# Performance work log

Measured on AMD Instinct MI355X. Metric: run time of the kernel, lower is better.

## Reference

```python
import jax, jax.numpy as jnp
import numpy as np

G = 8        # groups
GP = 8       # group_planes = out_planes // groups
K = 56       # kernel_size (attention axis length)
OP = 64      # out_planes
EPS = 1e-5   # BatchNorm eps (torch default)


def _bn(x, g, b, axes):
    # training-mode BatchNorm: batch statistics over `axes`, channel dim is axis 1
    m = x.mean(axes, keepdims=True)
    v = x.var(axes, keepdims=True)
    sh = [1] * x.ndim
    sh[1] = -1
    return (x - m) / jnp.sqrt(v + EPS) * g.reshape(sh) + b.reshape(sh)


def setup_inputs() -> dict:
    key = jax.random.key(0)
    k0, k1, k2 = jax.random.split(key, 3)
    x = jax.random.normal(k0, (1, 64, 32, 56, 32), jnp.float32)
    w_qkv = jax.random.normal(k1, (128, 64), jnp.float32) * (1.0 / 8.0)  # N(0, sqrt(1/in_planes))
    relative = jax.random.normal(k2, (16, 111), jnp.float32) * float(np.sqrt(1.0 / GP))
    return {
        "x": x,
        "w_qkv": w_qkv,
        "bn_qkv_g": jnp.ones(128, jnp.float32),
        "bn_qkv_b": jnp.zeros(128, jnp.float32),
        "bn_sim_g": jnp.ones(24, jnp.float32),
        "bn_sim_b": jnp.zeros(24, jnp.float32),
        "bn_out_g": jnp.ones(128, jnp.float32),
        "bn_out_b": jnp.zeros(128, jnp.float32),
        "relative": relative,
    }


def reference(x, w_qkv, bn_qkv_g, bn_qkv_b, bn_sim_g, bn_sim_b, bn_out_g, bn_out_b, relative):
    # get_input(x, 'x'): [N, C, D1, K, D2] -> [N, D1, D2, C, K]
    xp = jnp.transpose(x, (0, 2, 4, 1, 3))
    N, seq, W, C, Kk = xp.shape
    B = N * seq * W
    xb = xp.reshape(B, C, Kk)

    # 1x1 conv (qkv_transform) + BN1d
    qkv = jnp.einsum('oc,bck->bok', w_qkv, xb)            # [B, 2*OP, K]
    qkv = _bn(qkv, bn_qkv_g, bn_qkv_b, (0, 2))
    qkv = qkv.reshape(B, G, GP * 2, Kk)
    q, k, v = qkv[:, :, :GP // 2], qkv[:, :, GP // 2:GP], qkv[:, :, GP:]

    # relative position embeddings gathered from [2*GP, 2K-1] table
    qi = jnp.arange(K)[None, :]
    ki = jnp.arange(K)[:, None]
    flat = (ki - qi + K - 1).reshape(-1)
    emb = relative[:, flat].reshape(GP * 2, K, K)
    q_emb, k_emb, v_emb = emb[:GP // 2], emb[GP // 2:GP], emb[GP:]

    qr = jnp.einsum('bgci,cij->bgij', q, q_emb)
    kr = jnp.einsum('bgci,cij->bgij', k, k_emb).transpose(0, 1, 3, 2)
    qk = jnp.einsum('bgci,bgcj->bgij', q, k)

    ss = jnp.concatenate([qk, qr, kr], axis=1)            # [B, 3G, K, K]
    ss = _bn(ss, bn_sim_g, bn_sim_b, (0, 2, 3))
    sim = ss.reshape(B, 3, G, K, K).sum(axis=1)           # [B, G, K, K]
    sim = jax.nn.softmax(sim, axis=3)

    sv = jnp.einsum('bgij,bgcj->bgci', sim, v)            # [B, G, GP, K]
    sve = jnp.einsum('bgij,cij->bgci', sim, v_emb)        # [B, G, GP, K]
    so = jnp.concatenate([sv, sve], axis=-1).reshape(B, OP * 2, Kk)
    out = _bn(so, bn_out_g, bn_out_b, (0, 2))
    out = out.reshape(N, seq, W, OP, 2, Kk).sum(axis=-2)  # [N, seq, W, OP, K]

    # get_output(output, 'x'): [N, seq, W, OP, K] -> [N, OP, seq, K, W]
    return jnp.transpose(out, (0, 3, 1, 4, 2))
```

## Files before the change

### kernel.cpp

```cpp
#include <hip/hip_runtime.h>
#include <math.h>

#define EPS 1e-5f

typedef float f32x2 __attribute__((ext_vector_type(2)));
typedef float f32x4 __attribute__((ext_vector_type(4)));
__device__ __forceinline__ f32x2 fma2(f32x2 a, f32x2 b, f32x2 c) {
    return __builtin_elementwise_fma(a, b, c);
}
__device__ __forceinline__ f32x4 fma4(f32x4 a, f32x4 b, f32x4 c) {
    return __builtin_elementwise_fma(a, b, c);
}
__device__ __forceinline__ f32x2 sp2(float x) { f32x2 r = {x, x}; return r; }

__device__ __forceinline__ float dpp_add_shl(float v, int n) {
    int x;
    switch (n) {
        case 1: x = __builtin_amdgcn_mov_dpp(__float_as_int(v), 0x101, 0xF, 0xF, true); break;
        case 2: x = __builtin_amdgcn_mov_dpp(__float_as_int(v), 0x102, 0xF, 0xF, true); break;
        case 4: x = __builtin_amdgcn_mov_dpp(__float_as_int(v), 0x104, 0xF, 0xF, true); break;
        default: x = __builtin_amdgcn_mov_dpp(__float_as_int(v), 0x108, 0xF, 0xF, true); break;
    }
    return v + __int_as_float(x);
}
__device__ __forceinline__ float row_sum16(float v) {
    v = dpp_add_shl(v, 1);
    v = dpp_add_shl(v, 2);
    v = dpp_add_shl(v, 4);
    v = dpp_add_shl(v, 8);
    return v;
}


__global__ __launch_bounds__(256) void k_qkv2(const float* __restrict__ x,
                                              const float* __restrict__ w,
                                              const float* __restrict__ rel,
                                              float* __restrict__ qkv,
                                              float* __restrict__ P,
                                              float* __restrict__ tab) {
    __shared__ __align__(16) float X[64 * 256];
    __shared__ float T[8 * 264];
    const int t = threadIdx.x;

    if (blockIdx.x == 448) {
        float* r = X;
        for (int idx = t; idx < 444; idx += 256)
            *(float4*)&r[idx * 4] = *(const float4*)&rel[idx * 4];
        __syncthreads();
        for (int o = t; o < 2240; o += 256) {
            int row = o / 56, i = o - row * 56;
            float s = 0.f;
            if (row < 8) {
                const float* rr = &r[row * 111];
#pragma unroll
                for (int u = 0; u < 56; ++u) s += rr[i + u];
            } else if (row < 24) {
                int p = row - 8;
                const float* ra = &r[(p >> 2) * 111];
                const float* rb = &r[(p & 3) * 111];
#pragma unroll
                for (int u = 0; u < 56; ++u) s = fmaf(ra[i + u], rb[i + u], s);
            } else {
                int p = row - 24;
                const float* ra = &r[(4 + (p >> 2)) * 111];
                const float* rb = &r[(4 + (p & 3)) * 111];
#pragma unroll
                for (int u = 0; u < 56; ++u) s = fmaf(ra[i + u], rb[i + u], s);
            }
            tab[o] = s;
        }
        for (int o = t; o < 888; o += 256) {
            int c = o / 111, u = o - c * 111;
            tab[2240 + o] = rel[888 + c * 111 + 110 - u];
        }
        return;
    }

    const int tile = blockIdx.x % 224;
    const int half = blockIdx.x / 224;
    const int m0 = tile << 8;
    const int s = m0 / 1792;
    const int i0 = (m0 - s * 1792) >> 5;

    const float* xb = x + m0;
#pragma unroll
    for (int j = 0; j < 16; ++j) {
        int f = (j << 8) + t;
        int c = f >> 6, col = (f & 63) << 2;
        *(float4*)&X[(c << 8) + col] = *(const float4*)&xb[(size_t)c * 57344 + col];
    }
    __syncthreads();

    float* qb = qkv + (size_t)s * 229376 + i0;

    for (int oc = half * 8; oc < half * 8 + 8; ++oc) {
        const int o0 = oc << 3;
        const float* wp = w + (o0 << 6);
        f32x2 a01 = {0, 0}, a23 = {0, 0}, a45 = {0, 0}, a67 = {0, 0};
        for (int c = 0; c < 64; ++c) {
            float xv = X[(c << 8) + t];
            f32x2 w01 = {wp[c], wp[64 + c]};
            f32x2 w23 = {wp[128 + c], wp[192 + c]};
            f32x2 w45 = {wp[256 + c], wp[320 + c]};
            f32x2 w67 = {wp[384 + c], wp[448 + c]};
            f32x2 xs = sp2(xv);
            a01 = fma2(w01, xs, a01);
            a23 = fma2(w23, xs, a23);
            a45 = fma2(w45, xs, a45);
            a67 = fma2(w67, xs, a67);
        }
        float accv[8] = {a01.x, a01.y, a23.x, a23.y, a45.x, a45.y, a67.x, a67.y};
        __syncthreads();
#pragma unroll
        for (int k = 0; k < 8; ++k) T[k * 264 + t + (t >> 5)] = accv[k];
        __syncthreads();
#pragma unroll
        for (int e = 0; e < 8; ++e) {
            int flat = (e << 8) + t;
            int wcol = flat >> 6, oo = (flat >> 3) & 7, il = flat & 7;
            int mm = (il << 5) + wcol;
            qb[(size_t)wcol * 7168 + (o0 + oo) * 56 + il] = T[oo * 264 + mm + (mm >> 5)];
        }
        {
            int row = t >> 5, part = t & 31;
            float s1 = 0.f, s2 = 0.f;
#pragma unroll
            for (int e = 0; e < 8; ++e) {
                int mm = (part << 3) + e;
                float v = T[row * 264 + mm + (mm >> 5)];
                s1 += v; s2 += v * v;
            }
            s1 = row_sum16(s1);
            s2 = row_sum16(s2);
            s1 += __shfl_xor(s1, 16);
            s2 += __shfl_xor(s2, 16);
            if (part == 0) {
                P[(o0 + row) * 224 + tile] = s1;
                P[(128 + o0 + row) * 224 + tile] = s2;
            }
        }
    }
}

__global__ __launch_bounds__(256) void k_fin_red(const float* __restrict__ P,
                                                 const float* __restrict__ g,
                                                 const float* __restrict__ bb,
                                                 float* __restrict__ prm,
                                                 int nch, int npart, float invN) {
    __shared__ float rd[8];
    const int c = blockIdx.x, t = threadIdx.x;
    const float* r1 = P + (size_t)c * npart;
    const float* r2 = P + (size_t)(nch + c) * npart;
    float s1 = 0.f, s2 = 0.f;
    for (int p = t; p < npart; p += 256) { s1 += r1[p]; s2 += r2[p]; }
#pragma unroll
    for (int off = 32; off > 0; off >>= 1) { s1 += __shfl_xor(s1, off); s2 += __shfl_xor(s2, off); }
    if ((t & 63) == 0) { rd[t >> 6] = s1; rd[4 + (t >> 6)] = s2; }
    __syncthreads();
    if (t == 0) {
        s1 = rd[0] + rd[1] + rd[2] + rd[3];
        s2 = rd[4] + rd[5] + rd[6] + rd[7];
        float m = s1 * invN;
        float v = s2 * invN - m * m;
        float sc = g[c] * rsqrtf(v + EPS);
        prm[c] = sc;
        prm[nch + c] = bb[c] - m * sc;
    }
}

__global__ void k_fin(const float* __restrict__ sums, const float* __restrict__ g,
                      const float* __restrict__ bb, float* __restrict__ prm,
                      int nch, float invN) {
    int c = threadIdx.x;
    if (c >= nch) return;
    float m = sums[c] * invN;
    float v = sums[nch + c] * invN - m * m;
    float sc = g[c] * rsqrtf(v + EPS);
    prm[c] = sc;
    prm[nch + c] = bb[c] - m * sc;
}

__global__ __launch_bounds__(256) void k_sim3(const float* __restrict__ qkv,
                                              const float* __restrict__ prmQ,
                                              const float* __restrict__ tab,
                                              float* __restrict__ P) {
    __shared__ __align__(16) float qn[64 * 60];
    __shared__ __align__(16) float T[40 * 60];
    __shared__ float red[8 * 6];
    const int t = threadIdx.x, b = blockIdx.x;

    const float* span = qkv + (size_t)b * 7168;
    for (int idx = t; idx < 896; idx += 256) {
        int e0 = idx * 4;
        int g = e0 / 448, r = e0 - g * 448, c = r / 56, i = r - c * 56;
        int ch = g * 16 + c;
        float sc = prmQ[ch], sh = prmQ[128 + ch];
        float4 vv = *(const float4*)&span[g * 896 + r];
        float4 o;
        o.x = vv.x * sc + sh; o.y = vv.y * sc + sh;
        o.z = vv.z * sc + sh; o.w = vv.w * sc + sh;
        *(float4*)&qn[(g * 8 + c) * 60 + i] = o;
    }
    for (int idx = t; idx < 560; idx += 256) {
        int e0 = idx * 4;
        int row = e0 / 56, i = e0 - row * 56;
        int lr = (row < 8) ? (32 + row) : (row - 8);
        *(float4*)&T[lr * 60 + i] = *(const float4*)&tab[e0];
    }
    __syncthreads();

    const int g = t >> 5, u = t & 31;
    const int half = (u < 16) ? 0 : 4;
    const float* rowA = &qn[g * 480 + (half + ((u >> 2) & 3)) * 60];
    const float* rowB = &qn[g * 480 + (half + (u & 3)) * 60];
    const float* tabS = &T[u * 60];
    const float* tabR = &T[(32 + half + (u & 3)) * 60];

    f32x4 gram4 = {0, 0, 0, 0}, wgt4 = {0, 0, 0, 0};
    f32x4 lin14 = {0, 0, 0, 0}, lin24 = {0, 0, 0, 0};
#pragma unroll
    for (int i = 0; i < 56; i += 4) {
        f32x4 a = *(const f32x4*)&rowA[i];
        f32x4 b2 = *(const f32x4*)&rowB[i];
        f32x4 p = a * b2;
        gram4 += p;
        wgt4 = fma4(p, *(const f32x4*)&tabS[i], wgt4);
        lin14 += b2;
        lin24 = fma4(b2, *(const f32x4*)&tabR[i], lin24);
    }
    float gram = (gram4.x + gram4.y) + (gram4.z + gram4.w);
    float wgt = (wgt4.x + wgt4.y) + (wgt4.z + wgt4.w);
    float lin1 = (lin14.x + lin14.y) + (lin14.z + lin14.w);
    float lin2 = (lin24.x + lin24.y) + (lin24.z + lin24.w);

    float linP = __shfl_xor(lin1, 16);
    float gramP = __shfl_xor(gram, 16);
    float v0 = (u < 4) ? lin1 * linP : 0.f;
    float v1 = (u < 16) ? gram * gramP : 0.f;
    float v2 = (u < 4) ? lin2 : 0.f;
    float v3 = (u < 16) ? wgt : 0.f;
    float v4 = (u >= 16 && u < 20) ? lin2 : 0.f;
    float v5 = (u >= 16) ? wgt : 0.f;
    v0 = row_sum16(v0); v1 = row_sum16(v1); v2 = row_sum16(v2);
    v3 = row_sum16(v3); v4 = row_sum16(v4); v5 = row_sum16(v5);
    v0 += __shfl_xor(v0, 16); v1 += __shfl_xor(v1, 16);
    v2 += __shfl_xor(v2, 16); v3 += __shfl_xor(v3, 16);
    v4 += __shfl_xor(v4, 16); v5 += __shfl_xor(v5, 16);
    if (u == 0) {
        red[g * 6 + 0] = v0; red[g * 6 + 1] = v1; red[g * 6 + 2] = v2;
        red[g * 6 + 3] = v3; red[g * 6 + 4] = v4; red[g * 6 + 5] = v5;
    }
    __syncthreads();
    if (t < 48) {
        int g2 = t / 6, s = t - g2 * 6;
        int row = ((s & 1) ? 24 : 0) + (s >> 1) * 8 + g2;
        P[(size_t)row * 1024 + b] = red[g2 * 6 + s];
    }
}

__global__ __launch_bounds__(256) void k_main8(float* __restrict__ qkv,
                                               const float* __restrict__ rel,
                                               const float* __restrict__ tabrv,
                                               const float* __restrict__ prmQ,
                                               const float* __restrict__ prmS,
                                               float* __restrict__ P2,
                                               int useP2) {
    const int bg = blockIdx.x;
    const int g = bg & 7;
    __shared__ __align__(16) float S[16 * 60];
    __shared__ __align__(16) float rall[1776];
    __shared__ __align__(16) unsigned short Pms[56 * 72];
    __shared__ float red[128];

    const int t = threadIdx.x;
    float* span = qkv + (size_t)bg * 896;

    if (t < 224) {
        int e0 = t * 4;
        int c = e0 / 56, i = e0 - c * 56;
        int ch = g * 16 + c;
        float sc = prmQ[ch], sh = prmQ[128 + ch];
        float4 vv = *(const float4*)&span[e0];
        float4 o;
        o.x = vv.x * sc + sh; o.y = vv.y * sc + sh;
        o.z = vv.z * sc + sh; o.w = vv.w * sc + sh;
        *(float4*)&S[c * 60 + i] = o;
    }
    for (int idx = t; idx < 222; idx += 256)
        *(float4*)&rall[idx * 4] = *(const float4*)&rel[idx * 4];
    for (int idx = t; idx < 222; idx += 256)
        *(float4*)&rall[888 + idx * 4] = *(const float4*)&tabrv[idx * 4];
    __syncthreads();

    const int lane = t & 63, w = t >> 6;
    const int i_base = w * 14;
    const bool act = lane < 56;
    const int j = act ? lane : 0;

    const float k0 = S[240 + j], k1 = S[300 + j], k2 = S[360 + j], k3 = S[420 + j];
    const float LOG2E = 1.4426950408889634f;
    const float sc_qk = prmS[g] * LOG2E, sc_qr = prmS[8 + g] * LOG2E, sc_kr = prmS[16 + g] * LOG2E;

#pragma unroll 2
    for (int r = 0; r < 14; r += 2) {
        const int i0 = i_base + r;
        f32x2 q0 = *(const f32x2*)&S[i0];
        f32x2 q1 = *(const f32x2*)&S[60 + i0];
        f32x2 q2 = *(const f32x2*)&S[120 + i0];
        f32x2 q3 = *(const f32x2*)&S[180 + i0];
        const float* rq = &rall[i0 - j + 55];
        const float* rk = &rall[444 + j - i0 + 54];

        f32x2 qk = q0 * k0;
        qk = fma2(q1, sp2(k1), qk);
        qk = fma2(q2, sp2(k2), qk);
        qk = fma2(q3, sp2(k3), qk);

        f32x2 rq0 = {rq[0], rq[1]},     rq1 = {rq[111], rq[112]};
        f32x2 rq2 = {rq[222], rq[223]}, rq3 = {rq[333], rq[334]};
        f32x2 qr = q0 * rq0;
        qr = fma2(q1, rq1, qr);
        qr = fma2(q2, rq2, qr);
        qr = fma2(q3, rq3, qr);

        f32x2 rk0 = {rk[1], rk[0]},     rk1 = {rk[112], rk[111]};
        f32x2 rk2 = {rk[223], rk[222]}, rk3 = {rk[334], rk[333]};
        f32x2 kr = sp2(k0) * rk0;
        kr = fma2(sp2(k1), rk1, kr);
        kr = fma2(sp2(k2), rk2, kr);
        kr = fma2(sp2(k3), rk3, kr);

        f32x2 s = qk * sc_qk;
        s = fma2(qr, sp2(sc_qr), s);
        s = fma2(kr, sp2(sc_kr), s);
        float e0 = __builtin_amdgcn_exp2f(s.x);
        float e1 = __builtin_amdgcn_exp2f(s.y);
        if (act) {
            unsigned int b0 = __float_as_uint(e0);
            unsigned int b1 = __float_as_uint(e1);
            Pms[i0 * 72 + j] = (unsigned short)((b0 + 0x8000u) >> 16);
            Pms[(i0 + 1) * 72 + j] = (unsigned short)((b1 + 0x8000u) >> 16);
        }
    }

    const int il = lane & 15, cc = lane >> 4;
    const bool pact = il < 14;
    const int i = pact ? (i_base + il) : i_base;
    const int cA = cc, cB = cc + 4;

    const unsigned short* Pb = &Pms[i * 72];
    const float* vbA = &S[(8 + cA) * 60];
    const float* vbB = &S[(8 + cB) * 60];
    const float* rvA = &rall[888 + cA * 111 + 55 - i];
    const float* rvB = &rall[888 + cB * 111 + 55 - i];
    f32x4 svA = {0, 0, 0, 0}, sveA = {0, 0, 0, 0};
    f32x4 svB = {0, 0, 0, 0}, sveB = {0, 0, 0, 0};
    f32x4 rs4 = {0, 0, 0, 0};
    for (int jj = 0; jj < 56; jj += 8) {
        uint4 pu = *(const uint4*)&Pb[jj];
        f32x4 pa = {__uint_as_float(pu.x << 16), __uint_as_float(pu.x & 0xFFFF0000u),
                    __uint_as_float(pu.y << 16), __uint_as_float(pu.y & 0xFFFF0000u)};
        f32x4 pb = {__uint_as_float(pu.z << 16), __uint_as_float(pu.z & 0xFFFF0000u),
                    __uint_as_float(pu.w << 16), __uint_as_float(pu.w & 0xFFFF0000u)};
        f32x4 vA0 = *(const f32x4*)&vbA[jj],   vA1 = *(const f32x4*)&vbA[jj + 4];
        f32x4 vB0 = *(const f32x4*)&vbB[jj],   vB1 = *(const f32x4*)&vbB[jj + 4];
        f32x4 rA0 = {rvA[jj], rvA[jj + 1], rvA[jj + 2], rvA[jj + 3]};
        f32x4 rA1 = {rvA[jj + 4], rvA[jj + 5], rvA[jj + 6], rvA[jj + 7]};
        f32x4 rB0 = {rvB[jj], rvB[jj + 1], rvB[jj + 2], rvB[jj + 3]};
        f32x4 rB1 = {rvB[jj + 4], rvB[jj + 5], rvB[jj + 6], rvB[jj + 7]};
        svA = fma4(pa, vA0, svA);   svA = fma4(pb, vA1, svA);
        sveA = fma4(pa, rA0, sveA); sveA = fma4(pb, rA1, sveA);
        svB = fma4(pa, vB0, svB);   svB = fma4(pb, vB1, svB);
        sveB = fma4(pa, rB0, sveB); sveB = fma4(pb, rB1, sveB);
        rs4 += pa; rs4 += pb;
    }
    float rs = (rs4.x + rs4.y) + (rs4.z + rs4.w);
    float inv = __builtin_amdgcn_rcpf(rs);
    float sva = ((svA.x + svA.y) + (svA.z + svA.w)) * inv;
    float svea = ((sveA.x + sveA.y) + (sveA.z + sveA.w)) * inv;
    float svb = ((svB.x + svB.y) + (svB.z + svB.w)) * inv;
    float sveb = ((sveB.x + sveB.y) + (sveB.z + sveB.w)) * inv;
    if (pact) {
        span[(cA * 2) * 56 + i] = sva;
        span[(cA * 2 + 1) * 56 + i] = svea;
        span[(cB * 2) * 56 + i] = svb;
        span[(cB * 2 + 1) * 56 + i] = sveb;
    }
    float a0 = pact ? sva : 0.f,  a1 = pact ? sva * sva : 0.f;
    float a2 = pact ? svea : 0.f, a3 = pact ? svea * svea : 0.f;
    float a4 = pact ? svb : 0.f,  a5 = pact ? svb * svb : 0.f;
    float a6 = pact ? sveb : 0.f, a7 = pact ? sveb * sveb : 0.f;
    a0 = row_sum16(a0); a1 = row_sum16(a1); a2 = row_sum16(a2); a3 = row_sum16(a3);
    a4 = row_sum16(a4); a5 = row_sum16(a5); a6 = row_sum16(a6); a7 = row_sum16(a7);
    if (il == 0) {
        int baseA = cc * 16 + w;
        int baseB = (4 + cc) * 16 + w;
        red[baseA + 0]  = a0;  red[baseA + 4]  = a1;
        red[baseA + 8]  = a2;  red[baseA + 12] = a3;
        red[baseB + 0]  = a4;  red[baseB + 4]  = a5;
        red[baseB + 8]  = a6;  red[baseB + 12] = a7;
    }
    __syncthreads();
    if (useP2 && t < 32) {
        float s = red[t * 4] + red[t * 4 + 1] + red[t * 4 + 2] + red[t * 4 + 3];
        int pass = t >> 4, cc2 = (t >> 2) & 3, v = t & 3;
        int c = cc2 + (pass << 2);
        int ch = g * 16 + c * 2 + (v >> 1);
        int row = (v & 1) ? (128 + ch) : ch;
        P2[(size_t)row * 1024 + (bg >> 3)] = s;
    }
}

__global__ __launch_bounds__(256) void k_stats(const float* __restrict__ so,
                                               float* __restrict__ sums) {
    const int t = threadIdx.x;
    const int o = blockIdx.x >> 3;
    const int b0 = (blockIdx.x & 7) << 7;
    float s1 = 0.f, s2 = 0.f;
#pragma unroll
    for (int j = 0; j < 7; ++j) {
        int f = (j << 8) + t;
        int row = f / 14, q = f - row * 14;
        const float* src = so + ((size_t)(b0 + row) * 128 + o) * 56 + (q << 2);
        float4 v = *(const float4*)src;
        s1 += v.x + v.y + v.z + v.w;
        s2 += v.x * v.x + v.y * v.y + v.z * v.z + v.w * v.w;
    }
#pragma unroll
    for (int off = 32; off > 0; off >>= 1) { s1 += __shfl_xor(s1, off); s2 += __shfl_xor(s2, off); }
    if ((t & 63) == 0) { atomicAdd(&sums[o], s1); atomicAdd(&sums[128 + o], s2); }
}

__global__ __launch_bounds__(256) void k_out2(const float* __restrict__ so,
                                              const float* __restrict__ prmO,
                                              float* __restrict__ out) {
    __shared__ float L[128 * 61];
    const int t = threadIdx.x;
    const int s = blockIdx.x & 31;
    const int pc = blockIdx.x >> 5;
    const int o0 = pc << 2;
    const int p0 = pc << 1;

#pragma unroll
    for (int j = 0; j < 7; ++j) {
        int f = (j << 8) + t;
        int row = f / 14, q = f - row * 14;
        int ch = row >> 5, wcol = row & 31;
        const float* src = so + ((size_t)(s * 32 + wcol) * 128 + o0 + ch) * 56 + (q << 2);
        float4 v = *(const float4*)src;
        float* dst = &L[row * 61 + (q << 2)];
        dst[0] = v.x; dst[1] = v.y; dst[2] = v.z; dst[3] = v.w;
    }
    __syncthreads();
#pragma unroll
    for (int j = 0; j < 14; ++j) {
        int flat = (j << 8) + t;
        int wcol = flat & 31, r = flat >> 5;
        int i = r % 56, pp = r / 56;
        float v0 = L[((pp * 2) * 32 + wcol) * 61 + i];
        float v1 = L[((pp * 2 + 1) * 32 + wcol) * 61 + i];
        float sc0 = prmO[o0 + (pp << 1)],     sh0 = prmO[128 + o0 + (pp << 1)];
        float sc1 = prmO[o0 + (pp << 1) + 1], sh1 = prmO[128 + o0 + (pp << 1) + 1];
        out[(((size_t)(p0 + pp) * 32 + s) * 56 + i) * 32 + wcol] =
            v0 * sc0 + sh0 + v1 * sc1 + sh1;
    }
}

extern "C" void kernel_launch(void* const* d_in, const int* in_sizes, int n_in,
                              void* d_out, int out_size, void* d_ws, size_t ws_size,
                              hipStream_t stream) {
    const float* x     = (const float*)d_in[0];
    const float* w_qkv = (const float*)d_in[1];
    const float* g_qkv = (const float*)d_in[2];
    const float* b_qkv = (const float*)d_in[3];
    const float* g_sim = (const float*)d_in[4];
    const float* b_sim = (const float*)d_in[5];
    const float* g_out = (const float*)d_in[6];
    const float* b_out = (const float*)d_in[7];
    const float* rel   = (const float*)d_in[8];
    float* out = (float*)d_out;

    float* ws    = (float*)d_ws;
    float* qkv   = ws;
    float* Pq    = ws + 7340032;
    float* prm   = ws + 7397376;
    float* tab   = ws + 7397936;
    float* sumsO = ws + 7401064;
    float* P2    = ws + 7401472;
    const bool big = ws_size >= (size_t)(7401472 + 262144) * sizeof(float);

    k_qkv2<<<449, 256, 0, stream>>>(x, w_qkv, rel, qkv, Pq, tab);
    k_fin_red<<<128, 256, 0, stream>>>(Pq, g_qkv, b_qkv, prm, 128, 224, 1.f / 57344.f);
    k_sim3<<<1024, 256, 0, stream>>>(qkv, prm, tab, Pq);
    k_fin_red<<<24, 256, 0, stream>>>(Pq, g_sim, b_sim, prm + 256, 24, 1024, 1.f / 3211264.f);

    if (big) {
        k_main8<<<8192, 256, 0, stream>>>(qkv, rel, tab + 2240, prm, prm + 256, P2, 1);
        k_fin_red<<<128, 256, 0, stream>>>(P2, g_out, b_out, prm + 304, 128, 1024, 1.f / 57344.f);
    } else {
        hipMemsetAsync(sumsO, 0, 256 * sizeof(float), stream);
        k_main8<<<8192, 256, 0, stream>>>(qkv, rel, tab + 2240, prm, prm + 256, sumsO, 0);
        k_stats<<<1024, 256, 0, stream>>>(qkv, sumsO);
        k_fin<<<1, 128, 0, stream>>>(sumsO, g_out, b_out, prm + 304, 128, 1.f / 57344.f);
    }
    k_out2<<<1024, 256, 0, stream>>>(qkv, prm + 304, out);
}
```

Baseline: 113.6 us.

## Fold BatchNorm finalize reductions into producer kernels via last-block atomic counters

Removes the three separate k_fin_red launches. The qkv and sim BN statistics are now finalized by whichever block of the producer kernel increments an atomic counter last, using a threadfence-based last-block pattern. The output BN finalize is recomputed redundantly inside each k_out3 block for its four channels. A memset now also zeroes the counters every call, and the last-block tail serializes a small reduction at the end of each producer kernel.

```diff
diff --git a/kernel.cpp b/kernel.cpp
--- a/kernel.cpp
+++ b/kernel.cpp
@@ -37,9 +37,14 @@
                                               const float* __restrict__ rel,
                                               float* __restrict__ qkv,
                                               float* __restrict__ P,
-                                              float* __restrict__ tab) {
+                                              float* __restrict__ tab,
+                                              const float* __restrict__ gq,
+                                              const float* __restrict__ bq,
+                                              float* __restrict__ prm,
+                                              int* __restrict__ ctr) {
     __shared__ __align__(16) float X[64 * 256];
     __shared__ float T[8 * 264];
+    __shared__ int lastf;
     const int t = threadIdx.x;
 
     if (blockIdx.x == 448) {
@@ -140,31 +145,28 @@
             }
         }
     }
-}
-
-__global__ __launch_bounds__(256) void k_fin_red(const float* __restrict__ P,
-                                                 const float* __restrict__ g,
-                                                 const float* __restrict__ bb,
-                                                 float* __restrict__ prm,
-                                                 int nch, int npart, float invN) {
-    __shared__ float rd[8];
-    const int c = blockIdx.x, t = threadIdx.x;
-    const float* r1 = P + (size_t)c * npart;
-    const float* r2 = P + (size_t)(nch + c) * npart;
-    float s1 = 0.f, s2 = 0.f;
-    for (int p = t; p < npart; p += 256) { s1 += r1[p]; s2 += r2[p]; }
-#pragma unroll
-    for (int off = 32; off > 0; off >>= 1) { s1 += __shfl_xor(s1, off); s2 += __shfl_xor(s2, off); }
-    if ((t & 63) == 0) { rd[t >> 6] = s1; rd[4 + (t >> 6)] = s2; }
-    __syncthreads();
-    if (t == 0) {
-        s1 = rd[0] + rd[1] + rd[2] + rd[3];
-        s2 = rd[4] + rd[5] + rd[6] + rd[7];
-        float m = s1 * invN;
-        float v = s2 * invN - m * m;
-        float sc = g[c] * rsqrtf(v + EPS);
-        prm[c] = sc;
-        prm[nch + c] = bb[c] - m * sc;
+
+    __threadfence();
+    __syncthreads();
+    if (t == 0) lastf = (atomicAdd(ctr, 1) == 447);
+    __syncthreads();
+    if (!lastf) return;
+    __threadfence();
+    {
+        int c = t & 127, which = t >> 7;
+        const float* row = P + (size_t)(which * 128 + c) * 224;
+        f32x4 a4 = {0, 0, 0, 0};
+#pragma unroll
+        for (int p = 0; p < 56; ++p) a4 += *(const f32x4*)&row[p * 4];
+        X[t] = (a4.x + a4.y) + (a4.z + a4.w);
+        __syncthreads();
+        if (t < 128) {
+            float m = X[t] * (1.f / 57344.f);
+            float v = X[128 + t] * (1.f / 57344.f) - m * m;
+            float sc = gq[t] * rsqrtf(v + EPS);
+            prm[t] = sc;
+            prm[128 + t] = bq[t] - m * sc;
+        }
     }
 }
 
@@ -183,10 +185,16 @@
 __global__ __launch_bounds__(256) void k_sim3(const float* __restrict__ qkv,
                                               const float* __restrict__ prmQ,
                                               const float* __restrict__ tab,
-                                              float* __restrict__ P) {
+                                              float* __restrict__ P,
+                                              const float* __restrict__ gs,
+                                              const float* __restrict__ bs,
+                                              float* __restrict__ prmOut,
+                                              int* __restrict__ ctr) {
     __shared__ __align__(16) float qn[64 * 60];
     __shared__ __align__(16) float T[40 * 60];
     __shared__ float red[8 * 6];
+    __shared__ float rsf[48];
+    __shared__ int lastf;
     const int t = threadIdx.x, b = blockIdx.x;
 
     const float* span = qkv + (size_t)b * 7168;
@@ -255,6 +263,35 @@
         int g2 = t / 6, s = t - g2 * 6;
         int row = ((s & 1) ? 24 : 0) + (s >> 1) * 8 + g2;
         P[(size_t)row * 1024 + b] = red[g2 * 6 + s];
+    }
+
+    __threadfence();
+    __syncthreads();
+    if (t == 0) lastf = (atomicAdd(ctr, 1) == 1023);
+    __syncthreads();
+    if (!lastf) return;
+    __threadfence();
+    {
+        float s = 0.f;
+        if (t < 192) {
+            int row = t >> 2, q = t & 3;
+            const float* rp = P + (size_t)row * 1024 + q * 256;
+            f32x4 a4 = {0, 0, 0, 0};
+#pragma unroll
+            for (int p = 0; p < 64; ++p) a4 += *(const f32x4*)&rp[p * 4];
+            s = (a4.x + a4.y) + (a4.z + a4.w);
+        }
+        s = dpp_add_shl(s, 1);
+        s = dpp_add_shl(s, 2);
+        if (t < 192 && (t & 3) == 0) rsf[t >> 2] = s;
+        __syncthreads();
+        if (t < 24) {
+            float m = rsf[t] * (1.f / 3211264.f);
+            float v = rsf[24 + t] * (1.f / 3211264.f) - m * m;
+            float sc = gs[t] * rsqrtf(v + EPS);
+            prmOut[t] = sc;
+            prmOut[24 + t] = bs[t] - m * sc;
+        }
     }
 }
 
@@ -431,15 +468,49 @@
     if ((t & 63) == 0) { atomicAdd(&sums[o], s1); atomicAdd(&sums[128 + o], s2); }
 }
 
-__global__ __launch_bounds__(256) void k_out2(const float* __restrict__ so,
+__global__ __launch_bounds__(256) void k_out3(const float* __restrict__ so,
+                                              const float* __restrict__ P2,
                                               const float* __restrict__ prmO,
-                                              float* __restrict__ out) {
+                                              const float* __restrict__ gO,
+                                              const float* __restrict__ bO,
+                                              float* __restrict__ out,
+                                              int useP2) {
     __shared__ float L[128 * 61];
+    __shared__ float rsum[8];
+    __shared__ float pr[8];
     const int t = threadIdx.x;
     const int s = blockIdx.x & 31;
     const int pc = blockIdx.x >> 5;
     const int o0 = pc << 2;
     const int p0 = pc << 1;
+
+    if (useP2) {
+        int rr = t >> 5, l32 = t & 31;
+        int ch = o0 + (rr & 3);
+        int prow = (rr < 4) ? ch : (128 + ch);
+        const float* rp = P2 + (size_t)prow * 1024 + l32 * 32;
+        f32x4 a4 = {0, 0, 0, 0};
+#pragma unroll
+        for (int p = 0; p < 8; ++p) a4 += *(const f32x4*)&rp[p * 4];
+        float sv = (a4.x + a4.y) + (a4.z + a4.w);
+        sv = row_sum16(sv);
+        sv += __shfl_xor(sv, 16);
+        if (l32 == 0) rsum[rr] = sv;
+        __syncthreads();
+        if (t < 4) {
+            float m = rsum[t] * (1.f / 57344.f);
+            float v = rsum[4 + t] * (1.f / 57344.f) - m * m;
+            float sc = gO[o0 + t] * rsqrtf(v + EPS);
+            pr[t] = sc;
+            pr[4 + t] = bO[o0 + t] - m * sc;
+        }
+    } else {
+        if (t < 4) {
+            pr[t] = prmO[o0 + t];
+            pr[4 + t] = prmO[128 + o0 + t];
+        }
+    }
+    __syncthreads();
 
 #pragma unroll
     for (int j = 0; j < 7; ++j) {
@@ -459,8 +530,8 @@
         int i = r % 56, pp = r / 56;
         float v0 = L[((pp * 2) * 32 + wcol) * 61 + i];
         float v1 = L[((pp * 2 + 1) * 32 + wcol) * 61 + i];
-        float sc0 = prmO[o0 + (pp << 1)],     sh0 = prmO[128 + o0 + (pp << 1)];
-        float sc1 = prmO[o0 + (pp << 1) + 1], sh1 = prmO[128 + o0 + (pp << 1) + 1];
+        float sc0 = pr[(pp << 1)],     sh0 = pr[4 + (pp << 1)];
+        float sc1 = pr[(pp << 1) + 1], sh1 = pr[4 + (pp << 1) + 1];
         out[(((size_t)(p0 + pp) * 32 + s) * 56 + i) * 32 + wcol] =
             v0 * sc0 + sh0 + v1 * sc1 + sh1;
     }
@@ -486,22 +557,24 @@
     float* prm   = ws + 7397376;
     float* tab   = ws + 7397936;
     float* sumsO = ws + 7401064;
+    int*   ctrs  = (int*)(ws + 7401320);
     float* P2    = ws + 7401472;
     const bool big = ws_size >= (size_t)(7401472 + 262144) * sizeof(float);
 
-    k_qkv2<<<449, 256, 0, stream>>>(x, w_qkv, rel, qkv, Pq, tab);
-    k_fin_red<<<128, 256, 0, stream>>>(Pq, g_qkv, b_qkv, prm, 128, 224, 1.f / 57344.f);
-    k_sim3<<<1024, 256, 0, stream>>>(qkv, prm, tab, Pq);
-    k_fin_red<<<24, 256, 0, stream>>>(Pq, g_sim, b_sim, prm + 256, 24, 1024, 1.f / 3211264.f);
+    hipMemsetAsync(sumsO, 0, 258 * sizeof(float), stream);
+
+    k_qkv2<<<449, 256, 0, stream>>>(x, w_qkv, rel, qkv, Pq, tab,
+                                    g_qkv, b_qkv, prm, ctrs);
+    k_sim3<<<1024, 256, 0, stream>>>(qkv, prm, tab, Pq,
+                                     g_sim, b_sim, prm + 256, ctrs + 1);
 
     if (big) {
         k_main8<<<8192, 256, 0, stream>>>(qkv, rel, tab + 2240, prm, prm + 256, P2, 1);
-        k_fin_red<<<128, 256, 0, stream>>>(P2, g_out, b_out, prm + 304, 128, 1024, 1.f / 57344.f);
+        k_out3<<<1024, 256, 0, stream>>>(qkv, P2, prm + 304, g_out, b_out, out, 1);
     } else {
-        hipMemsetAsync(sumsO, 0, 256 * sizeof(float), stream);
         k_main8<<<8192, 256, 0, stream>>>(qkv, rel, tab + 2240, prm, prm + 256, sumsO, 0);
         k_stats<<<1024, 256, 0, stream>>>(qkv, sumsO);
         k_fin<<<1, 128, 0, stream>>>(sumsO, g_out, b_out, prm + 304, 128, 1.f / 57344.f);
-    }
-    k_out2<<<1024, 256, 0, stream>>>(qkv, prm + 304, out);
-}
+        k_out3<<<1024, 256, 0, stream>>>(qkv, P2, prm + 304, g_out, b_out, out, 0);
+    }
+}
```

Result: slower. 266.9 us (+135.0%).
